# Performance work log

Hardware: AMD Instinct MI355X
Metric: run time of the kernel (lower is better)

Reference implementation:

```python
import jax, jax.numpy as jnp
import numpy as np

NUM_BITS = 10
MEM_SIZE = 2 ** NUM_BITS  # 1024
HIDDEN = 1024
INPUT = 1024
BATCH = 16384
LN_EPS = 1e-5


def setup_inputs() -> dict:
    key = jax.random.key(0)
    ks = jax.random.split(key, 8)
    s = 0.02
    return {
        "x": jax.random.normal(ks[0], (BATCH, INPUT), jnp.float32),
        "h_prev": jax.random.normal(ks[1], (BATCH, HIDDEN), jnp.float32),
        "memory": jax.random.normal(ks[2], (MEM_SIZE, HIDDEN), jnp.float32),
        "W_w": jax.random.normal(ks[3], (HIDDEN, INPUT), jnp.float32) * s,
        "W_b": jnp.zeros((HIDDEN,), jnp.float32),
        "U_w": jax.random.normal(ks[4], (HIDDEN, HIDDEN), jnp.float32) * s,
        "U_b": jnp.zeros((HIDDEN,), jnp.float32),
        "Q_w": jax.random.normal(ks[5], (HIDDEN, HIDDEN), jnp.float32) * s,
        "Q_b": jnp.zeros((HIDDEN,), jnp.float32),
        "M_w": jax.random.normal(ks[6], (NUM_BITS, HIDDEN), jnp.float32) * s,
        "M_b": jnp.zeros((NUM_BITS,), jnp.float32),
        "ln_g": jnp.ones((HIDDEN,), jnp.float32),
        "ln_b": jnp.zeros((HIDDEN,), jnp.float32),
    }


def reference(x, h_prev, memory, W_w, W_b, U_w, U_b, Q_w, Q_b, M_w, M_b, ln_g, ln_b):
    # Binary address from h_prev (eval-mode hard threshold, non-differentiable)
    powers = jnp.asarray(2 ** np.arange(NUM_BITS - 1, -1, -1), dtype=x.dtype)  # [num_bits]
    logits = h_prev @ M_w.T + M_b                              # [B, num_bits]
    binary = (jax.nn.sigmoid(logits) > 0.5).astype(x.dtype)    # hard bits
    index = jnp.clip((binary * powers).sum(-1).astype(jnp.int32), 0, MEM_SIZE - 1)  # [B]
    h_mem = memory[index]                                      # gather [B, H]
    # Fused linear combine + LayerNorm + sigmoid
    pre = x @ W_w.T + W_b + h_prev @ U_w.T + U_b + h_mem @ Q_w.T + Q_b  # [B, H]
    mu = pre.mean(-1, keepdims=True)
    var = ((pre - mu) ** 2).mean(-1, keepdims=True)            # biased var (torch LN)
    norm = (pre - mu) * jax.lax.rsqrt(var + LN_EPS)
    return jax.nn.sigmoid(norm * ln_g + ln_b)                  # h_new [B, H]
```

## Files before the change

kernel.cpp:

```cpp
#include <hip/hip_runtime.h>

#define BATCH   16384
#define HIDDEN  1024
#define KDIM    3072
#define NBITS   10

#define BM 256
#define BN 256
#define BK 64
#define NT (KDIM / BK)

typedef __bf16 bf16x8 __attribute__((ext_vector_type(8)));
typedef float  f32x4  __attribute__((ext_vector_type(4)));

__device__ __forceinline__ unsigned short f2bf(float f) {
    unsigned int u = __float_as_uint(f);
    u += 0x7FFFu + ((u >> 16) & 1u);
    return (unsigned short)(u >> 16);
}

__device__ __forceinline__ void gload_lds16(const void* g, void* l) {
    __builtin_amdgcn_global_load_lds(
        (const __attribute__((address_space(1))) unsigned int*)g,
        (__attribute__((address_space(3))) unsigned int*)l,
        16, 0, 0);
}

__global__ void pack_b_kernel(const float* __restrict__ W,
                              const float* __restrict__ U,
                              const float* __restrict__ Q,
                              unsigned short* __restrict__ Bm) {
    int c = blockIdx.x * 256 + threadIdx.x;
    if (c >= (HIDDEN * KDIM) / 4) return;
    int n = c / (KDIM / 4);
    int k = (c % (KDIM / 4)) * 4;
    const float* src = (k < 1024) ? (W + (size_t)n * 1024 + k)
                     : (k < 2048) ? (U + (size_t)n * 1024 + (k - 1024))
                                  : (Q + (size_t)n * 1024 + (k - 2048));
    float4 v = *reinterpret_cast<const float4*>(src);
    ushort4 o;
    o.x = f2bf(v.x); o.y = f2bf(v.y); o.z = f2bf(v.z); o.w = f2bf(v.w);
    *reinterpret_cast<ushort4*>(Bm + (size_t)n * KDIM + k) = o;
}

__global__ __launch_bounds__(256) void build_a_kernel(
        const float* __restrict__ x,
        const float* __restrict__ h_prev,
        const float* __restrict__ memory,
        const float* __restrict__ M_w,
        const float* __restrict__ M_b,
        unsigned short* __restrict__ A) {
    int row  = (blockIdx.x * blockDim.x + threadIdx.x) >> 6;
    int lane = threadIdx.x & 63;
    if (row >= BATCH) return;

    const float4* hp = reinterpret_cast<const float4*>(h_prev + (size_t)row * HIDDEN);
    float4 hv[4];
#pragma unroll
    for (int i = 0; i < 4; ++i) hv[i] = hp[i * 64 + lane];

    int idx = 0;
#pragma unroll
    for (int j = 0; j < NBITS; ++j) {
        const float4* mp = reinterpret_cast<const float4*>(M_w + (size_t)j * HIDDEN);
        float s = 0.f;
#pragma unroll
        for (int i = 0; i < 4; ++i) {
            float4 m = mp[i * 64 + lane];
            s += hv[i].x * m.x + hv[i].y * m.y + hv[i].z * m.z + hv[i].w * m.w;
        }
#pragma unroll
        for (int off = 32; off >= 1; off >>= 1) s += __shfl_xor(s, off, 64);
        float logit = s + M_b[j];
        if (logit > 0.f) idx |= (1 << (NBITS - 1 - j));
    }

    unsigned short* arow = A + (size_t)row * KDIM;
    const float4* xp = reinterpret_cast<const float4*>(x + (size_t)row * HIDDEN);
    const float4* gp = reinterpret_cast<const float4*>(memory + (size_t)idx * HIDDEN);
#pragma unroll
    for (int i = 0; i < 4; ++i) {
        int off = i * 256 + lane * 4;
        float4 vx = xp[i * 64 + lane];
        ushort4 ox; ox.x = f2bf(vx.x); ox.y = f2bf(vx.y); ox.z = f2bf(vx.z); ox.w = f2bf(vx.w);
        *reinterpret_cast<ushort4*>(arow + off) = ox;

        ushort4 oh; oh.x = f2bf(hv[i].x); oh.y = f2bf(hv[i].y); oh.z = f2bf(hv[i].z); oh.w = f2bf(hv[i].w);
        *reinterpret_cast<ushort4*>(arow + 1024 + off) = oh;

        float4 vm = gp[i * 64 + lane];
        ushort4 om; om.x = f2bf(vm.x); om.y = f2bf(vm.y); om.z = f2bf(vm.z); om.w = f2bf(vm.w);
        *reinterpret_cast<ushort4*>(arow + 2048 + off) = om;
    }
}


__device__ __forceinline__ void stage_g(const unsigned short* __restrict__ src,
                                        int rowbase, int kt, int g,
                                        unsigned short* ldsTile, int t) {
    const int o      = g * 8192 + t * 16;
    const int row    = o >> 7;
    const int inner  = o & 127;
    const int sinner = inner ^ ((row & 7) << 4);
    const char* gp = reinterpret_cast<const char*>(
                         src + (size_t)(rowbase + row) * KDIM + kt * BK) + sinner;
    gload_lds16(gp, reinterpret_cast<char*>(ldsTile) + o);
}

__device__ __forceinline__ bf16x8 ldsfrag(const unsigned short* tile, int row,
                                          int kbyte_x_sw) {
    return *reinterpret_cast<const bf16x8*>(
        reinterpret_cast<const char*>(tile) + row * 128 + kbyte_x_sw);
}

#define BAR_IN()                                                     \
    do {                                                             \
        asm volatile("" ::: "memory");                               \
        __builtin_amdgcn_s_barrier();                                \
        asm volatile("s_waitcnt lgkmcnt(0)" ::: "memory");           \
        __builtin_amdgcn_sched_barrier(0);                           \
    } while (0)

#define BAR_OUT()                                                    \
    do {                                                             \
        __builtin_amdgcn_sched_barrier(0);                           \
        asm volatile("" ::: "memory");                               \
        __builtin_amdgcn_s_barrier();                                \
    } while (0)

#define MFMA_Q(MB, NB)                                                         \
    {                                                                          \
        __builtin_amdgcn_s_setprio(1);                                         \
        _Pragma("unroll") for (int m_ = 0; m_ < 4; ++m_)                       \
        _Pragma("unroll") for (int n_ = 0; n_ < 2; ++n_)                       \
        _Pragma("unroll") for (int kk_ = 0; kk_ < 2; ++kk_)                    \
            acc[(MB) + m_][(NB) + n_] =                                        \
                __builtin_amdgcn_mfma_f32_16x16x32_bf16(                       \
                    af[m_][kk_], bfr[(NB) + n_][kk_],                          \
                    acc[(MB) + m_][(NB) + n_], 0, 0, 0);                       \
        __builtin_amdgcn_s_setprio(0);                                         \
    }

__global__ __launch_bounds__(512, 2) void gemm_kernel(
        const unsigned short* __restrict__ A,
        const unsigned short* __restrict__ Bm,
        float* __restrict__ C) {
    __shared__ alignas(16) unsigned short lds[2][2][BM * BK];

    const int bid  = blockIdx.x;
    const int wgid = (bid & 7) * 32 + (bid >> 3);
    const int mblk = wgid >> 2;
    const int nblk = wgid & 3;

    const int t    = threadIdx.x;
    const int lane = t & 63;
    const int w    = t >> 6;
    const int wr   = w >> 2;
    const int wc   = w & 3;
    const int rr   = lane & 15;
    const int rq   = lane >> 4;
    const int sw   = (rr & 7) << 4;
    const int rqb  = rq * 16;
    const int wrb  = wr * 128;
    const int wcb  = wc * 64;

    const int arow = mblk * BM;
    const int brow = nblk * BN;

    f32x4 acc[8][4] = {};

    {
#pragma unroll
        for (int g = 0; g < 4; ++g) stage_g(A,  arow, 0, g, &lds[0][0][0], t);
#pragma unroll
        for (int g = 0; g < 4; ++g) stage_g(Bm, brow, 0, g, &lds[0][1][0], t);
#pragma unroll
        for (int g = 0; g < 4; ++g) stage_g(Bm, brow, 1, g, &lds[1][1][0], t);
#pragma unroll
        for (int g = 0; g < 2; ++g) stage_g(A,  arow, 1, g, &lds[1][0][0], t);
        asm volatile("s_waitcnt vmcnt(6)" ::: "memory");
        asm volatile("" ::: "memory");
        __builtin_amdgcn_s_barrier();
    }

    bf16x8 af[4][2];
    bf16x8 bfr[4][2];

#pragma unroll 2
    for (int kt = 0; kt < NT; ++kt) {
        const int c = kt & 1;
        const unsigned short* At = &lds[c][0][0];
        const unsigned short* Bt = &lds[c][1][0];
        unsigned short* nxA = &lds[c ^ 1][0][0];
        unsigned short* curA = &lds[c][0][0];
        unsigned short* curB = &lds[c][1][0];

#pragma unroll
        for (int m = 0; m < 4; ++m) {
            af[m][0] = ldsfrag(At, wrb + m * 16 + rr, (0  ) ^ sw);
            af[m][1] = ldsfrag(At, wrb + m * 16 + rr, (64 + rqb) ^ sw);
        }
#pragma unroll
        for (int m = 0; m < 4; ++m)
            af[m][0] = ldsfrag(At, wrb + m * 16 + rr, (rqb) ^ sw);
#pragma unroll
        for (int n = 0; n < 4; ++n) {
            bfr[n][0] = ldsfrag(Bt, wcb + n * 16 + rr, (rqb) ^ sw);
            bfr[n][1] = ldsfrag(Bt, wcb + n * 16 + rr, (64 + rqb) ^ sw);
        }
        if (kt + 1 < NT) {
            stage_g(A, arow, kt + 1, 2, nxA, t);
            stage_g(A, arow, kt + 1, 3, nxA, t);
        }
        BAR_IN();
        MFMA_Q(0, 0);
        BAR_OUT();

        BAR_IN();
        MFMA_Q(0, 2);
        BAR_OUT();

#pragma unroll
        for (int m = 0; m < 4; ++m) {
            af[m][0] = ldsfrag(At, wrb + 64 + m * 16 + rr, (rqb) ^ sw);
            af[m][1] = ldsfrag(At, wrb + 64 + m * 16 + rr, (64 + rqb) ^ sw);
        }
        if (kt + 2 < NT) {
            stage_g(Bm, brow, kt + 2, 0, curB, t);
            stage_g(Bm, brow, kt + 2, 1, curB, t);
        }
        BAR_IN();
        MFMA_Q(4, 0);
        BAR_OUT();

        if (kt + 2 < NT) {
            stage_g(Bm, brow, kt + 2, 2, curB, t);
            stage_g(Bm, brow, kt + 2, 3, curB, t);
            stage_g(A,  arow, kt + 2, 0, curA, t);
            stage_g(A,  arow, kt + 2, 1, curA, t);
        }
        BAR_IN();
        MFMA_Q(4, 2);
        __builtin_amdgcn_sched_barrier(0);
        if (kt < NT - 2) {
            asm volatile("s_waitcnt vmcnt(6)" ::: "memory");
        } else if (kt == NT - 2) {
            asm volatile("s_waitcnt vmcnt(0)" ::: "memory");
        }
        asm volatile("" ::: "memory");
        __builtin_amdgcn_s_barrier();
    }

#pragma unroll
    for (int mi = 0; mi < 8; ++mi) {
#pragma unroll
        for (int n = 0; n < 4; ++n) {
            const int gcol = nblk * BN + wcb + n * 16 + rr;
#pragma unroll
            for (int j = 0; j < 4; ++j) {
                const int grow = mblk * BM + wrb + mi * 16 + rq * 4 + j;
                C[(size_t)grow * HIDDEN + gcol] = acc[mi][n][j];
            }
        }
    }
}

__global__ __launch_bounds__(256) void ln_kernel(
        float* __restrict__ C,
        const float* __restrict__ W_b, const float* __restrict__ U_b,
        const float* __restrict__ Q_b, const float* __restrict__ ln_g,
        const float* __restrict__ ln_b) {
    const int row = blockIdx.x;
    const int t   = threadIdx.x;
    float4* rowp = reinterpret_cast<float4*>(C + (size_t)row * HIDDEN);

    float4 p  = rowp[t];
    float4 bw = reinterpret_cast<const float4*>(W_b)[t];
    float4 bu = reinterpret_cast<const float4*>(U_b)[t];
    float4 bq = reinterpret_cast<const float4*>(Q_b)[t];
    p.x += bw.x + bu.x + bq.x;
    p.y += bw.y + bu.y + bq.y;
    p.z += bw.z + bu.z + bq.z;
    p.w += bw.w + bu.w + bq.w;

    float s  = p.x + p.y + p.z + p.w;
    float sq = p.x * p.x + p.y * p.y + p.z * p.z + p.w * p.w;
#pragma unroll
    for (int off = 32; off >= 1; off >>= 1) {
        s  += __shfl_xor(s,  off, 64);
        sq += __shfl_xor(sq, off, 64);
    }
    __shared__ float red[8];
    const int lane = t & 63, w = t >> 6;
    if (lane == 0) { red[w] = s; red[4 + w] = sq; }
    __syncthreads();
    const float S    = red[0] + red[1] + red[2] + red[3];
    const float SQ   = red[4] + red[5] + red[6] + red[7];
    const float mean = S * (1.0f / HIDDEN);
    const float var  = SQ * (1.0f / HIDDEN) - mean * mean;
    const float rstd = rsqrtf(var + 1e-5f);

    float4 g = reinterpret_cast<const float4*>(ln_g)[t];
    float4 b = reinterpret_cast<const float4*>(ln_b)[t];
    float4 o;
    o.x = 1.f / (1.f + __expf(-((p.x - mean) * rstd * g.x + b.x)));
    o.y = 1.f / (1.f + __expf(-((p.y - mean) * rstd * g.y + b.y)));
    o.z = 1.f / (1.f + __expf(-((p.z - mean) * rstd * g.z + b.z)));
    o.w = 1.f / (1.f + __expf(-((p.w - mean) * rstd * g.w + b.w)));
    rowp[t] = o;
}

extern "C" void kernel_launch(void* const* d_in, const int* in_sizes, int n_in,
                              void* d_out, int out_size, void* d_ws, size_t ws_size,
                              hipStream_t stream) {
    const float* x      = (const float*)d_in[0];
    const float* h_prev = (const float*)d_in[1];
    const float* memory = (const float*)d_in[2];
    const float* W_w    = (const float*)d_in[3];
    const float* W_b    = (const float*)d_in[4];
    const float* U_w    = (const float*)d_in[5];
    const float* U_b    = (const float*)d_in[6];
    const float* Q_w    = (const float*)d_in[7];
    const float* Q_b    = (const float*)d_in[8];
    const float* M_w    = (const float*)d_in[9];
    const float* M_b    = (const float*)d_in[10];
    const float* ln_g   = (const float*)d_in[11];
    const float* ln_b   = (const float*)d_in[12];

    unsigned short* A  = (unsigned short*)d_ws;
    unsigned short* Bm = A + (size_t)BATCH * KDIM;
    float* pre = (float*)d_out;

    hipLaunchKernelGGL(pack_b_kernel, dim3((HIDDEN * KDIM / 4 + 255) / 256), dim3(256), 0, stream,
                       W_w, U_w, Q_w, Bm);
    hipLaunchKernelGGL(build_a_kernel, dim3(BATCH / 4), dim3(256), 0, stream,
                       x, h_prev, memory, M_w, M_b, A);
    hipLaunchKernelGGL(gemm_kernel, dim3((BATCH / BM) * (HIDDEN / BN)), dim3(512), 0, stream,
                       A, Bm, pre);
    hipLaunchKernelGGL(ln_kernel, dim3(BATCH), dim3(256), 0, stream,
                       pre, W_b, U_b, Q_b, ln_g, ln_b);
}
```

Baseline: 177.7 us.

## Precompute memory@Q^T table and gather it in LayerNorm instead of GEMM

The gathered memory rows times Q^T are replaced by a precomputed 1024x1024 table (memory @ Q^T), built with a small split-K MFMA kernel that accumulates through atomics. The LN kernel adds the table row chosen by the per-row index. This shrinks the main GEMM K dimension from 3072 to 2048 and removes the bf16 gather write in build_a. It adds a memset, an extra kernel with atomic adds, and a random-row gather in LN. A redundant duplicate LDS fragment load in the GEMM loop is also removed.

```diff
diff --git a/kernel.cpp b/kernel.cpp
--- a/kernel.cpp
+++ b/kernel.cpp
@@ -2,13 +2,14 @@
 
 #define BATCH   16384
 #define HIDDEN  1024
-#define KDIM    3072
+#define K2      2048
+#define MEMSZ   1024
 #define NBITS   10
 
 #define BM 256
 #define BN 256
 #define BK 64
-#define NT (KDIM / BK)
+#define NT (K2 / BK)
 
 typedef __bf16 bf16x8 __attribute__((ext_vector_type(8)));
 typedef float  f32x4  __attribute__((ext_vector_type(4)));
@@ -26,30 +27,104 @@
         16, 0, 0);
 }
 
-__global__ void pack_b_kernel(const float* __restrict__ W,
-                              const float* __restrict__ U,
-                              const float* __restrict__ Q,
-                              unsigned short* __restrict__ Bm) {
-    int c = blockIdx.x * 256 + threadIdx.x;
-    if (c >= (HIDDEN * KDIM) / 4) return;
-    int n = c / (KDIM / 4);
-    int k = (c % (KDIM / 4)) * 4;
-    const float* src = (k < 1024) ? (W + (size_t)n * 1024 + k)
-                     : (k < 2048) ? (U + (size_t)n * 1024 + (k - 1024))
-                                  : (Q + (size_t)n * 1024 + (k - 2048));
+__global__ void pack_kernel(const float* __restrict__ W,
+                            const float* __restrict__ U,
+                            const float* __restrict__ memory,
+                            const float* __restrict__ Q,
+                            unsigned short* __restrict__ Bm,
+                            unsigned short* __restrict__ Mem,
+                            unsigned short* __restrict__ Qb) {
+    int u = blockIdx.x * 256 + threadIdx.x;
+    const float* src;
+    unsigned short* dst;
+    if (u < 524288) {
+        int n = u >> 9;
+        int k = (u & 511) * 4;
+        src = (k < 1024) ? (W + (size_t)n * 1024 + k)
+                         : (U + (size_t)n * 1024 + (k - 1024));
+        dst = Bm + (size_t)n * K2 + k;
+    } else if (u < 786432) {
+        int f = (u - 524288) * 4;
+        src = memory + f;  dst = Mem + f;
+    } else if (u < 1048576) {
+        int f = (u - 786432) * 4;
+        src = Q + f;  dst = Qb + f;
+    } else return;
     float4 v = *reinterpret_cast<const float4*>(src);
     ushort4 o;
     o.x = f2bf(v.x); o.y = f2bf(v.y); o.z = f2bf(v.z); o.w = f2bf(v.w);
-    *reinterpret_cast<ushort4*>(Bm + (size_t)n * KDIM + k) = o;
+    *reinterpret_cast<ushort4*>(dst) = o;
+}
+
+__global__ __launch_bounds__(256) void mq_kernel(
+        const unsigned short* __restrict__ Mem,
+        const unsigned short* __restrict__ Qb,
+        float* __restrict__ MQ) {
+    __shared__ unsigned short As[128 * 64];
+    __shared__ unsigned short Bs[128 * 64];
+
+    const int ks = blockIdx.x >> 6;
+    const int mb = (blockIdx.x >> 3) & 7;
+    const int nb = blockIdx.x & 7;
+    const int t    = threadIdx.x;
+    const int lane = t & 63;
+    const int w    = t >> 6;
+    const int wr   = w >> 1, wc = w & 1;
+    const int rr   = lane & 15, rq = lane >> 4;
+    const int c8   = (t & 7) * 8;
+    const int srow = t >> 3;
+
+    f32x4 acc[4][4] = {};
+
+    for (int kt = 0; kt < 4; ++kt) {
+        const int k0 = ks * 256 + kt * 64;
+#pragma unroll
+        for (int i = 0; i < 4; ++i) {
+            int r = i * 32 + srow;
+            gload_lds16(Mem + (size_t)(mb * 128 + r) * 1024 + k0 + c8, As + i * 2048 + t * 8);
+            gload_lds16(Qb  + (size_t)(nb * 128 + r) * 1024 + k0 + c8, Bs + i * 2048 + t * 8);
+        }
+        __syncthreads();
+#pragma unroll
+        for (int kk = 0; kk < 2; ++kk) {
+            const int krd = kk * 32 + rq * 8;
+            bf16x8 af[4], bfv[4];
+#pragma unroll
+            for (int m = 0; m < 4; ++m)
+                af[m] = *reinterpret_cast<const bf16x8*>(As + (wr * 64 + m * 16 + rr) * 64 + krd);
+#pragma unroll
+            for (int n = 0; n < 4; ++n)
+                bfv[n] = *reinterpret_cast<const bf16x8*>(Bs + (wc * 64 + n * 16 + rr) * 64 + krd);
+#pragma unroll
+            for (int m = 0; m < 4; ++m)
+#pragma unroll
+                for (int n = 0; n < 4; ++n)
+                    acc[m][n] = __builtin_amdgcn_mfma_f32_16x16x32_bf16(
+                        af[m], bfv[n], acc[m][n], 0, 0, 0);
+        }
+        __syncthreads();
+    }
+
+#pragma unroll
+    for (int m = 0; m < 4; ++m)
+#pragma unroll
+        for (int n = 0; n < 4; ++n) {
+            int gcol = nb * 128 + wc * 64 + n * 16 + rr;
+#pragma unroll
+            for (int j = 0; j < 4; ++j) {
+                int grow = mb * 128 + wr * 64 + m * 16 + rq * 4 + j;
+                atomicAdd(&MQ[(size_t)grow * 1024 + gcol], acc[m][n][j]);
+            }
+        }
 }
 
 __global__ __launch_bounds__(256) void build_a_kernel(
         const float* __restrict__ x,
         const float* __restrict__ h_prev,
-        const float* __restrict__ memory,
         const float* __restrict__ M_w,
         const float* __restrict__ M_b,
-        unsigned short* __restrict__ A) {
+        unsigned short* __restrict__ A,
+        int* __restrict__ idxbuf) {
     int row  = (blockIdx.x * blockDim.x + threadIdx.x) >> 6;
     int lane = threadIdx.x & 63;
     if (row >= BATCH) return;
@@ -74,10 +149,10 @@
         float logit = s + M_b[j];
         if (logit > 0.f) idx |= (1 << (NBITS - 1 - j));
     }
-
-    unsigned short* arow = A + (size_t)row * KDIM;
+    if (lane == 0) idxbuf[row] = idx;
+
+    unsigned short* arow = A + (size_t)row * K2;
     const float4* xp = reinterpret_cast<const float4*>(x + (size_t)row * HIDDEN);
-    const float4* gp = reinterpret_cast<const float4*>(memory + (size_t)idx * HIDDEN);
 #pragma unroll
     for (int i = 0; i < 4; ++i) {
         int off = i * 256 + lane * 4;
@@ -87,10 +162,6 @@
 
         ushort4 oh; oh.x = f2bf(hv[i].x); oh.y = f2bf(hv[i].y); oh.z = f2bf(hv[i].z); oh.w = f2bf(hv[i].w);
         *reinterpret_cast<ushort4*>(arow + 1024 + off) = oh;
-
-        float4 vm = gp[i * 64 + lane];
-        ushort4 om; om.x = f2bf(vm.x); om.y = f2bf(vm.y); om.z = f2bf(vm.z); om.w = f2bf(vm.w);
-        *reinterpret_cast<ushort4*>(arow + 2048 + off) = om;
     }
 }
 
@@ -103,7 +174,7 @@
     const int inner  = o & 127;
     const int sinner = inner ^ ((row & 7) << 4);
     const char* gp = reinterpret_cast<const char*>(
-                         src + (size_t)(rowbase + row) * KDIM + kt * BK) + sinner;
+                         src + (size_t)(rowbase + row) * K2 + kt * BK) + sinner;
     gload_lds16(gp, reinterpret_cast<char*>(ldsTile) + o);
 }
 
@@ -191,18 +262,15 @@
         const int c = kt & 1;
         const unsigned short* At = &lds[c][0][0];
         const unsigned short* Bt = &lds[c][1][0];
-        unsigned short* nxA = &lds[c ^ 1][0][0];
+        unsigned short* nxA  = &lds[c ^ 1][0][0];
         unsigned short* curA = &lds[c][0][0];
         unsigned short* curB = &lds[c][1][0];
 
 #pragma unroll
         for (int m = 0; m < 4; ++m) {
-            af[m][0] = ldsfrag(At, wrb + m * 16 + rr, (0  ) ^ sw);
+            af[m][0] = ldsfrag(At, wrb + m * 16 + rr, (rqb) ^ sw);
             af[m][1] = ldsfrag(At, wrb + m * 16 + rr, (64 + rqb) ^ sw);
         }
-#pragma unroll
-        for (int m = 0; m < 4; ++m)
-            af[m][0] = ldsfrag(At, wrb + m * 16 + rr, (rqb) ^ sw);
 #pragma unroll
         for (int n = 0; n < 4; ++n) {
             bfr[n][0] = ldsfrag(Bt, wcb + n * 16 + rr, (rqb) ^ sw);
@@ -267,21 +335,26 @@
 
 __global__ __launch_bounds__(256) void ln_kernel(
         float* __restrict__ C,
+        const int* __restrict__ idxbuf,
+        const float* __restrict__ MQ,
         const float* __restrict__ W_b, const float* __restrict__ U_b,
         const float* __restrict__ Q_b, const float* __restrict__ ln_g,
         const float* __restrict__ ln_b) {
     const int row = blockIdx.x;
     const int t   = threadIdx.x;
+    const int midx = idxbuf[row];
     float4* rowp = reinterpret_cast<float4*>(C + (size_t)row * HIDDEN);
+    const float4* mqp = reinterpret_cast<const float4*>(MQ + (size_t)midx * HIDDEN);
 
     float4 p  = rowp[t];
+    float4 mq = mqp[t];
     float4 bw = reinterpret_cast<const float4*>(W_b)[t];
     float4 bu = reinterpret_cast<const float4*>(U_b)[t];
     float4 bq = reinterpret_cast<const float4*>(Q_b)[t];
-    p.x += bw.x + bu.x + bq.x;
-    p.y += bw.y + bu.y + bq.y;
-    p.z += bw.z + bu.z + bq.z;
-    p.w += bw.w + bu.w + bq.w;
+    p.x += mq.x + bw.x + bu.x + bq.x;
+    p.y += mq.y + bw.y + bu.y + bq.y;
+    p.z += mq.z + bw.z + bu.z + bq.z;
+    p.w += mq.w + bw.w + bu.w + bq.w;
 
     float s  = p.x + p.y + p.z + p.w;
     float sq = p.x * p.x + p.y * p.y + p.z * p.z + p.w * p.w;
@@ -327,16 +400,24 @@
     const float* ln_g   = (const float*)d_in[11];
     const float* ln_b   = (const float*)d_in[12];
 
-    unsigned short* A  = (unsigned short*)d_ws;
-    unsigned short* Bm = A + (size_t)BATCH * KDIM;
+    char* ws = (char*)d_ws;
+    unsigned short* A   = (unsigned short*)(ws);
+    unsigned short* Bm  = (unsigned short*)(ws + 67108864);
+    unsigned short* Mem = (unsigned short*)(ws + 71303168);
+    unsigned short* Qb  = (unsigned short*)(ws + 73400320);
+    float*          MQ  = (float*)         (ws + 75497472);
+    int*            idx = (int*)           (ws + 79691776);
     float* pre = (float*)d_out;
 
-    hipLaunchKernelGGL(pack_b_kernel, dim3((HIDDEN * KDIM / 4 + 255) / 256), dim3(256), 0, stream,
-                       W_w, U_w, Q_w, Bm);
+    hipLaunchKernelGGL(pack_kernel, dim3(4096), dim3(256), 0, stream,
+                       W_w, U_w, memory, Q_w, Bm, Mem, Qb);
+    hipMemsetAsync(MQ, 0, (size_t)MEMSZ * HIDDEN * sizeof(float), stream);
+    hipLaunchKernelGGL(mq_kernel, dim3(256), dim3(256), 0, stream,
+                       Mem, Qb, MQ);
     hipLaunchKernelGGL(build_a_kernel, dim3(BATCH / 4), dim3(256), 0, stream,
-                       x, h_prev, memory, M_w, M_b, A);
+                       x, h_prev, M_w, M_b, A, idx);
     hipLaunchKernelGGL(gemm_kernel, dim3((BATCH / BM) * (HIDDEN / BN)), dim3(512), 0, stream,
                        A, Bm, pre);
     hipLaunchKernelGGL(ln_kernel, dim3(BATCH), dim3(256), 0, stream,
-                       pre, W_b, U_b, Q_b, ln_g, ln_b);
-}
+                       pre, idx, MQ, W_b, U_b, Q_b, ln_g, ln_b);
+}
```

New measurement: 173.2 us. -2.6%, faster.
